# Kernel tuning notes

Hardware: AMD Instinct MI355X
Metric: run time of the kernel (lower is better)

## Reference

```python
import jax, jax.numpy as jnp
import numpy as np

N, E, D, ED, SH = 100000, 1600000, 64, 16, 9

# Real spherical harmonics l=0,1,2, 'integral' normalization (e3nn default),
# applied to unit direction vectors. Coefficients: 1/(2*sqrt(pi)), sqrt(3/4pi), etc.

def _sh(d):
    x, y, z = d[:, 0], d[:, 1], d[:, 2]
    return jnp.stack([
        jnp.full_like(x, 0.28209479177387814),          # l=0
        0.4886025119029199 * y,                          # l=1, m=-1
        0.4886025119029199 * z,                          # l=1, m=0
        0.4886025119029199 * x,                          # l=1, m=1
        1.0925484305920792 * x * y,                      # l=2, m=-2
        1.0925484305920792 * y * z,                      # l=2, m=-1
        0.31539156525252005 * (3.0 * z * z - 1.0),       # l=2, m=0
        1.0925484305920792 * x * z,                      # l=2, m=1
        0.5462742152960396 * (x * x - y * y),            # l=2, m=2
    ], axis=1)


def _mlp(h, W1, b1, W2, b2):  # Linear -> SiLU -> Linear
    return jax.nn.silu(h @ W1 + b1) @ W2 + b2


def setup_inputs() -> dict:
    key = jax.random.key(0)
    ks = jax.random.split(key, 16)
    def rn(k, shape, scale=0.05):
        return jax.random.normal(k, shape, dtype=jnp.float32) * scale
    return {
        "x": jax.random.normal(ks[0], (N, D), jnp.float32),
        "pos": jax.random.normal(ks[1], (N, 3), jnp.float32) * 3.0,
        "edge_attr": jax.random.normal(ks[2], (E, ED), jnp.float32),
        "row": jax.random.randint(ks[3], (E,), 0, N, dtype=jnp.int32),
        "col": jax.random.randint(ks[4], (E,), 0, N, dtype=jnp.int32),
        "node_W1": rn(ks[5], (D, D)), "node_b1": jnp.zeros((D,), jnp.float32),
        "node_W2": rn(ks[6], (D, D)), "node_b2": jnp.zeros((D,), jnp.float32),
        "edge_W1": rn(ks[7], (SH + ED, D)), "edge_b1": jnp.zeros((D,), jnp.float32),
        "edge_W2": rn(ks[8], (D, D)), "edge_b2": jnp.zeros((D,), jnp.float32),
        "out_W1": rn(ks[9], (2 * D, D)), "out_b1": jnp.zeros((D,), jnp.float32),
        "out_W2": rn(ks[10], (D, D)), "out_b2": jnp.zeros((D,), jnp.float32),
        "bn_gamma": jnp.ones((D,), jnp.float32), "bn_beta": jnp.zeros((D,), jnp.float32),
    }


def reference(x, pos, edge_attr, row, col,
              node_W1, node_b1, node_W2, node_b2,
              edge_W1, edge_b1, edge_W2, edge_b2,
              out_W1, out_b1, out_W2, out_b2,
              bn_gamma, bn_beta):
    # gather node positions per edge -> relative vectors
    rel = pos[row] - pos[col]                                    # [E,3]
    length = jnp.sqrt(jnp.sum(rel * rel, axis=1, keepdims=True) + 1e-12)
    d = rel / length
    d = d / (jnp.sqrt(jnp.sum(d * d, axis=1, keepdims=True)) + 1e-10)
    edge_sh = _sh(d)                                             # [E,9]
    edge_feat = jnp.concatenate([edge_sh, edge_attr], axis=1)    # [E,9+ED]
    x_t = _mlp(x, node_W1, node_b1, node_W2, node_b2)            # [N,D]
    e_w = _mlp(edge_feat, edge_W1, edge_b1, edge_W2, edge_b2)    # [E,D]
    msg = x_t[row] * e_w                                         # message = x_j * edge_attr
    # scatter-mean onto target nodes (edge_index[1] == col)
    s = jax.ops.segment_sum(msg, col, num_segments=N)            # [N,D]
    cnt = jax.ops.segment_sum(jnp.ones((E,), msg.dtype), col, num_segments=N)
    agg = s / jnp.maximum(cnt, 1.0)[:, None]
    h = jnp.concatenate([agg, x], axis=1)                        # [N,2D]
    h = _mlp(h, out_W1, out_b1, out_W2, out_b2)                  # [N,D]
    # BatchNorm over node dim (scalar irreps), training-mode batch stats
    mean = jnp.mean(h, axis=0)
    var = jnp.var(h, axis=0)
    return (h - mean) / jnp.sqrt(var + 1e-5) * bn_gamma + bn_beta
```

## Files before the change

kernel.cpp:

```cpp
#include <hip/hip_runtime.h>
#include <math.h>

#define DD 64
#define EDA 16

#define FR_E1 0
#define FR_E2 4
#define FR_N1 12
#define FR_N2 20
#define FR_O1 28
#define FR_O2 44
#define FR_TOT 52

#define PADH 72
#define PADF 68

#define HS 72

typedef unsigned int u32;
typedef unsigned long long u64;
typedef __attribute__((ext_vector_type(8))) short short8;
typedef __attribute__((ext_vector_type(4))) float f32x4;

static __device__ __forceinline__ float silu(float v) {
    return v / (1.0f + __expf(-v));
}
static __device__ __forceinline__ unsigned short f2bf(float f) {
    unsigned u = __float_as_uint(f);
    unsigned r = u + 0x7FFFu + ((u >> 16) & 1u);
    return (unsigned short)(r >> 16);
}
static __device__ __forceinline__ float bf2f(unsigned short u) {
    return __uint_as_float(((unsigned)u) << 16);
}
static __device__ __forceinline__ float bflo(u32 v) {
    return __uint_as_float(v << 16);
}
static __device__ __forceinline__ float bfhi(u32 v) {
    return __uint_as_float(v & 0xFFFF0000u);
}
static __device__ __forceinline__ unsigned cvt_pk_bf16(float lo, float hi) {
    unsigned r;
    asm("v_cvt_pk_bf16_f32 %0, %1, %2" : "=v"(r) : "v"(lo), "v"(hi));
    return r;
}
static __device__ __forceinline__ int bperm(int idx_lane, int v) {
    return __builtin_amdgcn_ds_bpermute(idx_lane << 2, v);
}
static __device__ __forceinline__ void wave_lds_fence() {
    asm volatile("s_waitcnt lgkmcnt(0)" ::: "memory");
    __builtin_amdgcn_sched_barrier(0);
}

__global__ __launch_bounds__(256) void k_pack_w(
    const float* __restrict__ eW1, const float* __restrict__ eW2,
    const float* __restrict__ nW1, const float* __restrict__ nW2,
    const float* __restrict__ oW1, const float* __restrict__ oW2,
    unsigned short* __restrict__ wpk)
{
    int t = threadIdx.x;
    int nt = t >> 6, l = t & 63;
    int kc = l >> 4, n0 = l & 15;

    #pragma unroll
    for (int j = 0; j < 8; ++j) {
        int k = kc*8 + j;
        int orig = (k < 16) ? (9 + k) : ((k < 25) ? (k - 16) : -1);
        float v = (orig >= 0) ? eW1[orig*DD + nt*16 + n0] : 0.0f;
        wpk[((size_t)((FR_E1 + nt)*64 + l))*8 + j] = f2bf(v);
    }
    #pragma unroll
    for (int s = 0; s < 2; ++s) {
        #pragma unroll
        for (int j = 0; j < 8; ++j) {
            int k = s*32 + kc*8 + j;
            wpk[((size_t)((FR_E2 + s*4 + nt)*64 + l))*8 + j] = f2bf(eW2[k*DD + nt*16 + n0]);
            wpk[((size_t)((FR_N1 + s*4 + nt)*64 + l))*8 + j] = f2bf(nW1[k*DD + nt*16 + n0]);
            wpk[((size_t)((FR_N2 + s*4 + nt)*64 + l))*8 + j] = f2bf(nW2[k*DD + nt*16 + n0]);
            wpk[((size_t)((FR_O2 + s*4 + nt)*64 + l))*8 + j] = f2bf(oW2[k*DD + nt*16 + n0]);
        }
    }
    #pragma unroll
    for (int s = 0; s < 4; ++s) {
        #pragma unroll
        for (int j = 0; j < 8; ++j) {
            int k = s*32 + kc*8 + j;
            wpk[((size_t)((FR_O1 + s*4 + nt)*64 + l))*8 + j] = f2bf(oW1[k*DD + nt*16 + n0]);
        }
    }
}

__global__ __launch_bounds__(256, 2) void k_node_hist(
    const float* __restrict__ x,
    const unsigned short* __restrict__ wpk,
    const float* __restrict__ b1, const float* __restrict__ b2,
    unsigned short* __restrict__ x_tb, int n, int nodeBlocks,
    const int* __restrict__ col, u32* __restrict__ cnt, int n_e)
{
    __shared__ __align__(16) unsigned short tile[4][16*PADH];
    const int tid  = threadIdx.x;

    if (blockIdx.x >= nodeBlocks) {
        int g = (blockIdx.x - nodeBlocks) * 256 + tid;
        int base = g * 4;
        if (base + 3 < n_e) {
            int4 c = ((const int4*)col)[g];
            atomicAdd(&cnt[c.x], 1u);
            atomicAdd(&cnt[c.y], 1u);
            atomicAdd(&cnt[c.z], 1u);
            atomicAdd(&cnt[c.w], 1u);
        } else {
            for (int e = base; e < n_e; ++e) atomicAdd(&cnt[col[e]], 1u);
        }
        return;
    }

    const int wv   = tid >> 6;
    const int lane = tid & 63;
    const int kc   = lane >> 4;
    const int n0   = lane & 15;
    const int rbase = kc * 4;

    const short8* fb = (const short8*)wpk;
    short8 bw1[2][4], bw2[2][4];
    #pragma unroll
    for (int s = 0; s < 2; ++s)
        #pragma unroll
        for (int nt = 0; nt < 4; ++nt) {
            bw1[s][nt] = fb[(FR_N1 + s*4 + nt)*64 + lane];
            bw2[s][nt] = fb[(FR_N2 + s*4 + nt)*64 + lane];
        }
    float b1v[4], b2v[4];
    #pragma unroll
    for (int nt = 0; nt < 4; ++nt) { b1v[nt] = b1[nt*16 + n0]; b2v[nt] = b2[nt*16 + n0]; }

    const int base = blockIdx.x*64 + wv*16;
    int rc = min(base + n0, n - 1);
    const float* xr = x + (size_t)rc * DD;

    short8 a[2];
    #pragma unroll
    for (int m = 0; m < 2; ++m) {
        float4 u0 = *(const float4*)(xr + m*32 + kc*8);
        float4 u1 = *(const float4*)(xr + m*32 + kc*8 + 4);
        unsigned* au = (unsigned*)&a[m];
        au[0] = cvt_pk_bf16(u0.x, u0.y);
        au[1] = cvt_pk_bf16(u0.z, u0.w);
        au[2] = cvt_pk_bf16(u1.x, u1.y);
        au[3] = cvt_pk_bf16(u1.z, u1.w);
    }

    f32x4 zz = {0.f, 0.f, 0.f, 0.f};
    f32x4 hacc[4] = {zz, zz, zz, zz};
    #pragma unroll
    for (int m = 0; m < 2; ++m)
        #pragma unroll
        for (int nt = 0; nt < 4; ++nt)
            hacc[nt] = __builtin_amdgcn_mfma_f32_16x16x32_bf16(a[m], bw1[m][nt], hacc[nt], 0, 0, 0);

    #pragma unroll
    for (int nt = 0; nt < 4; ++nt)
        #pragma unroll
        for (int r = 0; r < 4; ++r)
            tile[wv][(rbase + r)*PADH + nt*16 + n0] = f2bf(silu(hacc[nt][r] + b1v[nt]));
    __syncthreads();

    short8 a2_0 = *(const short8*)&tile[wv][n0*PADH +  0 + kc*8];
    short8 a2_1 = *(const short8*)&tile[wv][n0*PADH + 32 + kc*8];
    f32x4 oacc[4];
    #pragma unroll
    for (int nt = 0; nt < 4; ++nt) {
        oacc[nt] = __builtin_amdgcn_mfma_f32_16x16x32_bf16(a2_0, bw2[0][nt], zz, 0, 0, 0);
        oacc[nt] = __builtin_amdgcn_mfma_f32_16x16x32_bf16(a2_1, bw2[1][nt], oacc[nt], 0, 0, 0);
    }
    __syncthreads();

    #pragma unroll
    for (int nt = 0; nt < 4; ++nt)
        #pragma unroll
        for (int r = 0; r < 4; ++r)
            tile[wv][(rbase + r)*PADH + nt*16 + n0] = f2bf(oacc[nt][r] + b2v[nt]);
    __syncthreads();

    int ei = lane >> 2, q = lane & 3;
    int er = base + ei;
    if (er < n) {
        uint4* dst = (uint4*)(x_tb + (size_t)er * DD);
        dst[q]     = *(const uint4*)&tile[wv][ei*PADH + q*8];
        dst[q + 4] = *(const uint4*)&tile[wv][ei*PADH + (q + 4)*8];
    }
}

__global__ __launch_bounds__(256) void k_scan1(
    const u32* __restrict__ cnt, u32* __restrict__ bsum, int n)
{
    __shared__ u32 s[256];
    int i = blockIdx.x * 256 + threadIdx.x;
    s[threadIdx.x] = (i < n) ? cnt[i] : 0u;
    __syncthreads();
    for (int o = 128; o > 0; o >>= 1) {
        if (threadIdx.x < o) s[threadIdx.x] += s[threadIdx.x + o];
        __syncthreads();
    }
    if (threadIdx.x == 0) bsum[blockIdx.x] = s[0];
}

__global__ __launch_bounds__(512) void k_scan2(
    const u32* __restrict__ bsum, u32* __restrict__ boff, int nb)
{
    __shared__ u32 s[512];
    int t = threadIdx.x;
    u32 v = (t < nb) ? bsum[t] : 0u;
    s[t] = v;
    __syncthreads();
    for (int o = 1; o < 512; o <<= 1) {
        u32 a = (t >= o) ? s[t - o] : 0u;
        __syncthreads();
        s[t] += a;
        __syncthreads();
    }
    if (t < nb) boff[t] = s[t] - v;
}

__global__ __launch_bounds__(256) void k_scan3(
    const u32* __restrict__ cnt, const u32* __restrict__ boff,
    u32* __restrict__ wp, int n)
{
    __shared__ u32 s[256];
    int t = threadIdx.x;
    int i = blockIdx.x * 256 + t;
    u32 v = (i < n) ? cnt[i] : 0u;
    s[t] = v;
    __syncthreads();
    for (int o = 1; o < 256; o <<= 1) {
        u32 a = (t >= o) ? s[t - o] : 0u;
        __syncthreads();
        s[t] += a;
        __syncthreads();
    }
    if (i < n) wp[i] = boff[blockIdx.x] + s[t] - v;
}

__global__ __launch_bounds__(256) void k_scatter(
    const int* __restrict__ row, const int* __restrict__ col,
    u32* __restrict__ wp, u64* __restrict__ ce,
    float* __restrict__ agg, int n_agg4, int n_e)
{
    int e = blockIdx.x * 256 + threadIdx.x;
    if (e < n_agg4) {
        float4 z = {0.f, 0.f, 0.f, 0.f};
        ((float4*)agg)[e] = z;
    }
    if (e >= n_e) return;
    int c = col[e];
    int r = row[e];
    u32 p = atomicAdd(&wp[c], 1u);
    u32 lo = (u32)e | ((u32)r << 21);
    u32 hi = ((u32)r >> 11) | ((u32)c << 6);
    u64 pk = (u64)lo | ((u64)hi << 32);
    __builtin_nontemporal_store(pk, &ce[p]);
}

__global__ __launch_bounds__(256, 4) void k_edge_fused(
    const float* __restrict__ pos,
    const float* __restrict__ edge_attr,
    const u64* __restrict__ ce,
    const unsigned short* __restrict__ x_tb,
    const unsigned short* __restrict__ wpk,
    const float* __restrict__ b1, const float* __restrict__ b2,
    float* __restrict__ agg, int n_e)
{
    __shared__ __align__(16) unsigned short t_s[4][16*HS];
    __shared__ __align__(16) unsigned short wls[8*64*8];

    const int tid  = threadIdx.x;
    const int wv   = tid >> 6;
    const int lane = tid & 63;
    const int kc   = lane >> 4;
    const int n0   = lane & 15;

    {
        const uint4* wsrc = (const uint4*)(wpk + FR_E2*64*8);
        uint4* wdst = (uint4*)wls;
        wdst[tid*2]     = wsrc[tid*2];
        wdst[tid*2 + 1] = wsrc[tid*2 + 1];
    }

    const short8* fb = (const short8*)wpk;
    short8 bw1[4];
    #pragma unroll
    for (int nt = 0; nt < 4; ++nt) bw1[nt] = fb[(FR_E1 + nt)*64 + lane];

    uint2 bp1[4], bp2[4];
    #pragma unroll
    for (int nt = 0; nt < 4; ++nt) {
        float4 q1 = *(const float4*)(b1 + nt*16 + kc*4);
        float4 q2 = *(const float4*)(b2 + nt*16 + kc*4);
        bp1[nt].x = cvt_pk_bf16(q1.x, q1.y); bp1[nt].y = cvt_pk_bf16(q1.z, q1.w);
        bp2[nt].x = cvt_pk_bf16(q2.x, q2.y); bp2[nt].y = cvt_pk_bf16(q2.z, q2.w);
    }

    const int gbase = blockIdx.x*256 + wv*64;
    int g  = gbase + lane;
    int gc = min(g, n_e - 1);
    u64 pk = ce[gc];
    u32 pklo = (u32)pk, pkhi = (u32)(pk >> 32);
    int eo = (int)(pklo & 0x1FFFFFu);
    int rw = (int)((pklo >> 21) | ((pkhi & 0x3Fu) << 11));
    int cl = (int)(pkhi >> 6);

    float ax = pos[3*rw+0] - pos[3*cl+0];
    float ay = pos[3*rw+1] - pos[3*cl+1];
    float az = pos[3*rw+2] - pos[3*cl+2];
    float len = sqrtf(fmaf(ax,ax, fmaf(ay,ay, az*az)) + 1e-12f);
    float dx = ax/len, dy = ay/len, dz = az/len;
    float n2 = sqrtf(fmaf(dx,dx, fmaf(dy,dy, dz*dz)));
    float inv = 1.0f/(n2 + 1e-10f);
    dx *= inv; dy *= inv; dz *= inv;

    u32 shp01 = cvt_pk_bf16(0.28209479177387814f, 0.4886025119029199f*dy);
    u32 shp23 = cvt_pk_bf16(0.4886025119029199f*dz, 0.4886025119029199f*dx);
    u32 shp45 = cvt_pk_bf16(1.0925484305920792f*dx*dy, 1.0925484305920792f*dy*dz);
    u32 shp67 = cvt_pk_bf16(0.31539156525252005f*(3.0f*dz*dz - 1.0f),
                            1.0925484305920792f*dx*dz);
    u32 shp8  = cvt_pk_bf16(0.5462742152960396f*(dx*dx - dy*dy), 0.0f);

    int cln = bperm(min(lane + 1, 63), cl);
    u64 fmask = __ballot(cln != cl) | 0x8000800080008000ull;

    f32x4 zz = {0.f, 0.f, 0.f, 0.f};

    __syncthreads();

    #pragma unroll 1
    for (int tt = 0; tt < 4; ++tt) {
        const int le = tt*16 + n0;
        bool valid = (gbase + le) < n_e;

        int ea  = bperm(le, eo);
        int rv  = bperm(le, rw);
        u32 s01 = (u32)bperm(le, (int)shp01);
        u32 s23 = (u32)bperm(le, (int)shp23);
        u32 s45 = (u32)bperm(le, (int)shp45);
        u32 s67 = (u32)bperm(le, (int)shp67);
        u32 s8  = (u32)bperm(le, (int)shp8);

        const unsigned short* xrow = x_tb + (size_t)rv * DD;
        uint2 xv0 = *(const uint2*)(xrow +  0 + kc*4);
        uint2 xv1 = *(const uint2*)(xrow + 16 + kc*4);
        uint2 xv2 = *(const uint2*)(xrow + 32 + kc*4);
        uint2 xv3 = *(const uint2*)(xrow + 48 + kc*4);

        short8 af;
        unsigned* au = (unsigned*)&af;
        if (kc < 2) {
            const float4* ap = (const float4*)(edge_attr + (size_t)ea*EDA + kc*8);
            float4 a0 = ap[0], a1 = ap[1];
            au[0] = cvt_pk_bf16(a0.x, a0.y);
            au[1] = cvt_pk_bf16(a0.z, a0.w);
            au[2] = cvt_pk_bf16(a1.x, a1.y);
            au[3] = cvt_pk_bf16(a1.z, a1.w);
        } else if (kc == 2) {
            au[0] = s01; au[1] = s23; au[2] = s45; au[3] = s67;
        } else {
            au[0] = s8; au[1] = 0u; au[2] = 0u; au[3] = 0u;
        }

        f32x4 hacc[4];
        #pragma unroll
        for (int nt = 0; nt < 4; ++nt)
            hacc[nt] = __builtin_amdgcn_mfma_f32_16x16x32_bf16(bw1[nt], af, zz, 0, 0, 0);

        #pragma unroll
        for (int nt = 0; nt < 4; ++nt) {
            float h0 = silu(hacc[nt][0] + bflo(bp1[nt].x));
            float h1 = silu(hacc[nt][1] + bfhi(bp1[nt].x));
            float h2 = silu(hacc[nt][2] + bflo(bp1[nt].y));
            float h3 = silu(hacc[nt][3] + bfhi(bp1[nt].y));
            uint2 pr;
            pr.x = cvt_pk_bf16(h0, h1);
            pr.y = cvt_pk_bf16(h2, h3);
            *(uint2*)&t_s[wv][n0*HS + nt*16 + kc*4] = pr;
        }
        wave_lds_fence();

        short8 bf0 = *(const short8*)&t_s[wv][n0*HS +  0 + kc*8];
        short8 bf1 = *(const short8*)&t_s[wv][n0*HS + 32 + kc*8];
        f32x4 oacc[4];
        #pragma unroll
        for (int nt = 0; nt < 4; ++nt) {
            short8 w0 = *(const short8*)&wls[((0*4 + nt)*64 + lane)*8];
            oacc[nt] = __builtin_amdgcn_mfma_f32_16x16x32_bf16(w0, bf0, zz, 0, 0, 0);
            short8 w1 = *(const short8*)&wls[((1*4 + nt)*64 + lane)*8];
            oacc[nt] = __builtin_amdgcn_mfma_f32_16x16x32_bf16(w1, bf1, oacc[nt], 0, 0, 0);
        }

        if (!valid) {
            xv0.x = xv0.y = xv1.x = xv1.y = 0u;
            xv2.x = xv2.y = xv3.x = xv3.y = 0u;
        }
        {
            float m0, m1, m2, m3;
            uint2 pr;
            m0 = (oacc[0][0] + bflo(bp2[0].x)) * bflo(xv0.x);
            m1 = (oacc[0][1] + bfhi(bp2[0].x)) * bfhi(xv0.x);
            m2 = (oacc[0][2] + bflo(bp2[0].y)) * bflo(xv0.y);
            m3 = (oacc[0][3] + bfhi(bp2[0].y)) * bfhi(xv0.y);
            pr.x = cvt_pk_bf16(m0, m1); pr.y = cvt_pk_bf16(m2, m3);
            *(uint2*)&t_s[wv][n0*HS +  0 + kc*4] = pr;
            m0 = (oacc[1][0] + bflo(bp2[1].x)) * bflo(xv1.x);
            m1 = (oacc[1][1] + bfhi(bp2[1].x)) * bfhi(xv1.x);
            m2 = (oacc[1][2] + bflo(bp2[1].y)) * bflo(xv1.y);
            m3 = (oacc[1][3] + bfhi(bp2[1].y)) * bfhi(xv1.y);
            pr.x = cvt_pk_bf16(m0, m1); pr.y = cvt_pk_bf16(m2, m3);
            *(uint2*)&t_s[wv][n0*HS + 16 + kc*4] = pr;
            m0 = (oacc[2][0] + bflo(bp2[2].x)) * bflo(xv2.x);
            m1 = (oacc[2][1] + bfhi(bp2[2].x)) * bfhi(xv2.x);
            m2 = (oacc[2][2] + bflo(bp2[2].y)) * bflo(xv2.y);
            m3 = (oacc[2][3] + bfhi(bp2[2].y)) * bfhi(xv2.y);
            pr.x = cvt_pk_bf16(m0, m1); pr.y = cvt_pk_bf16(m2, m3);
            *(uint2*)&t_s[wv][n0*HS + 32 + kc*4] = pr;
            m0 = (oacc[3][0] + bflo(bp2[3].x)) * bflo(xv3.x);
            m1 = (oacc[3][1] + bfhi(bp2[3].x)) * bfhi(xv3.x);
            m2 = (oacc[3][2] + bflo(bp2[3].y)) * bflo(xv3.y);
            m3 = (oacc[3][3] + bfhi(bp2[3].y)) * bfhi(xv3.y);
            pr.x = cvt_pk_bf16(m0, m1); pr.y = cvt_pk_bf16(m2, m3);
            *(uint2*)&t_s[wv][n0*HS + 48 + kc*4] = pr;
        }
        wave_lds_fence();

        {
            float acc = 0.0f;
            #pragma unroll
            for (int r = 0; r < 16; ++r) {
                acc += bf2f(t_s[wv][r*HS + lane]);
                if ((fmask >> (tt*16 + r)) & 1ull) {
                    int cur = __builtin_amdgcn_readlane(cl, tt*16 + r);
                    unsafeAtomicAdd(&agg[(size_t)cur*DD + lane], acc);
                    acc = 0.0f;
                }
            }
        }
    }
}

__global__ __launch_bounds__(256, 2) void k_out_mfma(
    const float* __restrict__ agg, const u32* __restrict__ cnt,
    const float* __restrict__ x,
    const unsigned short* __restrict__ wpk,
    const float* __restrict__ b1, const float* __restrict__ b2,
    float* __restrict__ h, float* __restrict__ sums, int n)
{
    __shared__ __align__(16) unsigned short htile[4][16*PADH];
    __shared__ __align__(16) float otile[4][16*PADF];
    const int tid  = threadIdx.x;
    const int wv   = tid >> 6;
    const int lane = tid & 63;
    const int kc   = lane >> 4;
    const int n0   = lane & 15;
    const int rbase = kc * 4;

    const short8* fb = (const short8*)wpk;
    short8 bw1[4][4], bw2[2][4];
    #pragma unroll
    for (int s = 0; s < 4; ++s)
        #pragma unroll
        for (int nt = 0; nt < 4; ++nt) bw1[s][nt] = fb[(FR_O1 + s*4 + nt)*64 + lane];
    #pragma unroll
    for (int s = 0; s < 2; ++s)
        #pragma unroll
        for (int nt = 0; nt < 4; ++nt) bw2[s][nt] = fb[(FR_O2 + s*4 + nt)*64 + lane];

    float b1v[4], b2v[4];
    #pragma unroll
    for (int nt = 0; nt < 4; ++nt) { b1v[nt] = b1[nt*16 + n0]; b2v[nt] = b2[nt*16 + n0]; }

    const int base = blockIdx.x*64 + wv*16;
    int rc = min(base + n0, n - 1);
    const float* ar = agg + (size_t)rc * DD;
    const float* xr = x   + (size_t)rc * DD;
    float invc = 1.0f / fmaxf((float)cnt[rc], 1.0f);

    short8 a[4];
    #pragma unroll
    for (int m = 0; m < 4; ++m) {
        const float* src = (m < 2) ? (ar + m*32 + kc*8) : (xr + (m-2)*32 + kc*8);
        float4 u0 = *(const float4*)(src);
        float4 u1 = *(const float4*)(src + 4);
        if (m < 2) {
            u0.x*=invc; u0.y*=invc; u0.z*=invc; u0.w*=invc;
            u1.x*=invc; u1.y*=invc; u1.z*=invc; u1.w*=invc;
        }
        unsigned* au = (unsigned*)&a[m];
        au[0] = cvt_pk_bf16(u0.x, u0.y);
        au[1] = cvt_pk_bf16(u0.z, u0.w);
        au[2] = cvt_pk_bf16(u1.x, u1.y);
        au[3] = cvt_pk_bf16(u1.z, u1.w);
    }

    f32x4 zz = {0.f, 0.f, 0.f, 0.f};
    f32x4 hacc[4] = {zz, zz, zz, zz};
    #pragma unroll
    for (int m = 0; m < 4; ++m)
        #pragma unroll
        for (int nt = 0; nt < 4; ++nt)
            hacc[nt] = __builtin_amdgcn_mfma_f32_16x16x32_bf16(a[m], bw1[m][nt], hacc[nt], 0, 0, 0);

    #pragma unroll
    for (int nt = 0; nt < 4; ++nt)
        #pragma unroll
        for (int r = 0; r < 4; ++r)
            htile[wv][(rbase + r)*PADH + nt*16 + n0] = f2bf(silu(hacc[nt][r] + b1v[nt]));
    __syncthreads();

    short8 a2_0 = *(const short8*)&htile[wv][n0*PADH +  0 + kc*8];
    short8 a2_1 = *(const short8*)&htile[wv][n0*PADH + 32 + kc*8];
    f32x4 oacc[4];
    #pragma unroll
    for (int nt = 0; nt < 4; ++nt) {
        oacc[nt] = __builtin_amdgcn_mfma_f32_16x16x32_bf16(a2_0, bw2[0][nt], zz, 0, 0, 0);
        oacc[nt] = __builtin_amdgcn_mfma_f32_16x16x32_bf16(a2_1, bw2[1][nt], oacc[nt], 0, 0, 0);
    }

    #pragma unroll
    for (int nt = 0; nt < 4; ++nt)
        #pragma unroll
        for (int r = 0; r < 4; ++r)
            otile[wv][(rbase + r)*PADF + nt*16 + n0] = oacc[nt][r] + b2v[nt];
    __syncthreads();

    int ei = lane >> 2, q = lane & 3;
    int er = base + ei;
    if (er < n) {
        float4* dst = (float4*)(h + (size_t)er * DD);
        #pragma unroll
        for (int k = 0; k < 4; ++k)
            dst[q + 4*k] = *(const float4*)&otile[wv][ei*PADF + (q + 4*k)*4];
    }

    if (tid < 64) {
        int f = tid;
        float s = 0.f, qq = 0.f;
        #pragma unroll
        for (int w = 0; w < 4; ++w) {
            int base_w = blockIdx.x*64 + w*16;
            int nv = n - base_w;
            nv = nv < 0 ? 0 : (nv > 16 ? 16 : nv);
            for (int r = 0; r < nv; ++r) {
                float v = otile[w][r*PADF + f];
                s += v; qq = fmaf(v, v, qq);
            }
        }
        unsafeAtomicAdd(&sums[f], s);
        unsafeAtomicAdd(&sums[DD + f], qq);
    }
}

__global__ __launch_bounds__(256) void k_bn_norm(
    float* __restrict__ h, const float* __restrict__ sums,
    const float* __restrict__ gamma, const float* __restrict__ beta,
    float inv_n, int total4)
{
    int g = blockIdx.x*256 + threadIdx.x;
    if (g >= total4) return;
    int f0 = (g*4) & (DD-1);
    float4 v = ((const float4*)h)[g];
    float4 sm = *(const float4*)(sums + f0);
    float4 sq = *(const float4*)(sums + DD + f0);
    float4 gm = *(const float4*)(gamma + f0);
    float4 bt = *(const float4*)(beta + f0);
    float m0 = sm.x*inv_n, m1 = sm.y*inv_n, m2 = sm.z*inv_n, m3 = sm.w*inv_n;
    float s0 = gm.x * rsqrtf(sq.x*inv_n - m0*m0 + 1e-5f);
    float s1 = gm.y * rsqrtf(sq.y*inv_n - m1*m1 + 1e-5f);
    float s2 = gm.z * rsqrtf(sq.z*inv_n - m2*m2 + 1e-5f);
    float s3 = gm.w * rsqrtf(sq.w*inv_n - m3*m3 + 1e-5f);
    v.x = fmaf(v.x - m0, s0, bt.x);
    v.y = fmaf(v.y - m1, s1, bt.y);
    v.z = fmaf(v.z - m2, s2, bt.z);
    v.w = fmaf(v.w - m3, s3, bt.w);
    ((float4*)h)[g] = v;
}

static inline size_t al16(size_t v) { return (v + 15) & ~(size_t)15; }

extern "C" void kernel_launch(void* const* d_in, const int* in_sizes, int n_in,
                              void* d_out, int out_size, void* d_ws, size_t ws_size,
                              hipStream_t stream)
{
    const float* x         = (const float*)d_in[0];
    const float* pos       = (const float*)d_in[1];
    const float* edge_attr = (const float*)d_in[2];
    const int*   row       = (const int*)d_in[3];
    const int*   col       = (const int*)d_in[4];
    const float* nW1 = (const float*)d_in[5];
    const float* nb1 = (const float*)d_in[6];
    const float* nW2 = (const float*)d_in[7];
    const float* nb2 = (const float*)d_in[8];
    const float* eW1 = (const float*)d_in[9];
    const float* eb1 = (const float*)d_in[10];
    const float* eW2 = (const float*)d_in[11];
    const float* eb2 = (const float*)d_in[12];
    const float* oW1 = (const float*)d_in[13];
    const float* ob1 = (const float*)d_in[14];
    const float* oW2 = (const float*)d_in[15];
    const float* ob2 = (const float*)d_in[16];
    const float* gamma = (const float*)d_in[17];
    const float* beta  = (const float*)d_in[18];

    const int N = in_sizes[0] / DD;
    const int E = in_sizes[3];
    const int NB = (N + 255) / 256;
    const int nodeBlocks = (N + 63) / 64;
    const int histBlocks = (E/4 + 255) / 256;

    float* hout = (float*)d_out;
    char* ws = (char*)d_ws;

    size_t o_xtb  = 0;
    size_t o_cnt  = o_xtb  + (size_t)N*DD*2;
    size_t o_sums = o_cnt  + (size_t)N*4;
    size_t o_agg  = o_sums + 128*4;
    size_t o_wp   = o_agg  + (size_t)N*DD*4;
    size_t o_bsum = o_wp   + (size_t)N*4;
    size_t o_boff = al16(o_bsum + (size_t)NB*4);
    size_t o_wpk  = al16(o_boff + (size_t)NB*4);
    size_t o_ce   = al16(o_wpk + (size_t)FR_TOT*64*8*2);
    size_t need   = o_ce + (size_t)E*8;

    if (ws_size < need) return;

    unsigned short* x_tb = (unsigned short*)(ws + o_xtb);
    u32*   cnt  = (u32*)(ws + o_cnt);
    float* sums = (float*)(ws + o_sums);
    float* agg  = (float*)(ws + o_agg);
    u32*   wp   = (u32*)(ws + o_wp);
    u32*   bsum = (u32*)(ws + o_bsum);
    u32*   boff = (u32*)(ws + o_boff);
    unsigned short* wpk = (unsigned short*)(ws + o_wpk);
    u64*   ce   = (u64*)(ws + o_ce);

    hipMemsetAsync(cnt, 0, (size_t)N*4 + 128*4, stream);

    k_pack_w<<<1, 256, 0, stream>>>(eW1, eW2, nW1, nW2, oW1, oW2, wpk);
    k_node_hist<<<nodeBlocks + histBlocks, 256, 0, stream>>>(
        x, wpk, nb1, nb2, x_tb, N, nodeBlocks, col, cnt, E);
    k_scan1<<<NB, 256, 0, stream>>>(cnt, bsum, N);
    k_scan2<<<1, 512, 0, stream>>>(bsum, boff, NB);
    k_scan3<<<NB, 256, 0, stream>>>(cnt, boff, wp, N);
    k_scatter<<<(E + 255)/256, 256, 0, stream>>>(row, col, wp, ce, agg, N*DD/4, E);
    k_edge_fused<<<(E + 255)/256, 256, 0, stream>>>(pos, edge_attr, ce, x_tb,
                                                    wpk, eb1, eb2, agg, E);
    k_out_mfma<<<(N + 63)/64, 256, 0, stream>>>(agg, cnt, x, wpk, ob1, ob2, hout, sums, N);
    k_bn_norm<<<(N*DD/4 + 255)/256, 256, 0, stream>>>(hout, sums, gamma, beta,
                                                      1.0f/(float)N, N*DD/4);
}
```

Before: 337.8 us.

## Collapse scan kernels into one atomic-offset scan, fold memset into pack kernel

Replaces the three-kernel exclusive scan with a single kernel in which each block claims its base offset from a global atomic counter. The resulting segment offsets are not in node order, which is acceptable for bucketing edges by destination. The memset is folded into the weight-pack kernel as extra zeroing blocks, removing launches and serialization. The x_t row layout is permuted so the edge kernel can read each node row with two 16-byte loads instead of four 8-byte loads. The node kernel's occupancy hint is also raised to 3 blocks per multiprocessor.

```diff
diff --git a/kernel.cpp b/kernel.cpp
--- a/kernel.cpp
+++ b/kernel.cpp
@@ -52,12 +52,18 @@
     __builtin_amdgcn_sched_barrier(0);
 }
 
-__global__ __launch_bounds__(256) void k_pack_w(
+__global__ __launch_bounds__(256) void k_pack_zero(
     const float* __restrict__ eW1, const float* __restrict__ eW2,
     const float* __restrict__ nW1, const float* __restrict__ nW2,
     const float* __restrict__ oW1, const float* __restrict__ oW2,
-    unsigned short* __restrict__ wpk)
-{
+    unsigned short* __restrict__ wpk,
+    uint4* __restrict__ zbase, int nz4)
+{
+    if (blockIdx.x > 0) {
+        int i = (blockIdx.x - 1) * 256 + threadIdx.x;
+        if (i < nz4) zbase[i] = make_uint4(0u, 0u, 0u, 0u);
+        return;
+    }
     int t = threadIdx.x;
     int nt = t >> 6, l = t & 63;
     int kc = l >> 4, n0 = l & 15;
@@ -90,7 +96,7 @@
     }
 }
 
-__global__ __launch_bounds__(256, 2) void k_node_hist(
+__global__ __launch_bounds__(256, 3) void k_node_hist(
     const float* __restrict__ x,
     const unsigned short* __restrict__ wpk,
     const float* __restrict__ b1, const float* __restrict__ b2,
@@ -179,7 +185,8 @@
     for (int nt = 0; nt < 4; ++nt)
         #pragma unroll
         for (int r = 0; r < 4; ++r)
-            tile[wv][(rbase + r)*PADH + nt*16 + n0] = f2bf(oacc[nt][r] + b2v[nt]);
+            tile[wv][(rbase + r)*PADH + (n0>>2)*16 + nt*4 + (n0&3)] =
+                f2bf(oacc[nt][r] + b2v[nt]);
     __syncthreads();
 
     int ei = lane >> 2, q = lane & 3;
@@ -191,42 +198,12 @@
     }
 }
 
-__global__ __launch_bounds__(256) void k_scan1(
-    const u32* __restrict__ cnt, u32* __restrict__ bsum, int n)
+__global__ __launch_bounds__(256) void k_scan_bump(
+    const u32* __restrict__ cnt, u32* __restrict__ wp,
+    u32* __restrict__ gctr, int n)
 {
     __shared__ u32 s[256];
-    int i = blockIdx.x * 256 + threadIdx.x;
-    s[threadIdx.x] = (i < n) ? cnt[i] : 0u;
-    __syncthreads();
-    for (int o = 128; o > 0; o >>= 1) {
-        if (threadIdx.x < o) s[threadIdx.x] += s[threadIdx.x + o];
-        __syncthreads();
-    }
-    if (threadIdx.x == 0) bsum[blockIdx.x] = s[0];
-}
-
-__global__ __launch_bounds__(512) void k_scan2(
-    const u32* __restrict__ bsum, u32* __restrict__ boff, int nb)
-{
-    __shared__ u32 s[512];
-    int t = threadIdx.x;
-    u32 v = (t < nb) ? bsum[t] : 0u;
-    s[t] = v;
-    __syncthreads();
-    for (int o = 1; o < 512; o <<= 1) {
-        u32 a = (t >= o) ? s[t - o] : 0u;
-        __syncthreads();
-        s[t] += a;
-        __syncthreads();
-    }
-    if (t < nb) boff[t] = s[t] - v;
-}
-
-__global__ __launch_bounds__(256) void k_scan3(
-    const u32* __restrict__ cnt, const u32* __restrict__ boff,
-    u32* __restrict__ wp, int n)
-{
-    __shared__ u32 s[256];
+    __shared__ u32 base;
     int t = threadIdx.x;
     int i = blockIdx.x * 256 + t;
     u32 v = (i < n) ? cnt[i] : 0u;
@@ -238,7 +215,9 @@
         s[t] += a;
         __syncthreads();
     }
-    if (i < n) wp[i] = boff[blockIdx.x] + s[t] - v;
+    if (t == 255) base = atomicAdd(gctr, s[255]);
+    __syncthreads();
+    if (i < n) wp[i] = base + s[t] - v;
 }
 
 __global__ __launch_bounds__(256) void k_scatter(
@@ -345,11 +324,11 @@
         u32 s67 = (u32)bperm(le, (int)shp67);
         u32 s8  = (u32)bperm(le, (int)shp8);
 
-        const unsigned short* xrow = x_tb + (size_t)rv * DD;
-        uint2 xv0 = *(const uint2*)(xrow +  0 + kc*4);
-        uint2 xv1 = *(const uint2*)(xrow + 16 + kc*4);
-        uint2 xv2 = *(const uint2*)(xrow + 32 + kc*4);
-        uint2 xv3 = *(const uint2*)(xrow + 48 + kc*4);
+        const unsigned short* xrow = x_tb + (size_t)rv * DD + kc*16;
+        uint4 qa = *(const uint4*)(xrow);
+        uint4 qb = *(const uint4*)(xrow + 8);
+        uint2 xv0 = {qa.x, qa.y}, xv1 = {qa.z, qa.w};
+        uint2 xv2 = {qb.x, qb.y}, xv3 = {qb.z, qb.w};
 
         short8 af;
         unsigned* au = (unsigned*)&af;
@@ -619,11 +598,10 @@
     size_t o_xtb  = 0;
     size_t o_cnt  = o_xtb  + (size_t)N*DD*2;
     size_t o_sums = o_cnt  + (size_t)N*4;
-    size_t o_agg  = o_sums + 128*4;
+    size_t o_gctr = o_sums + 128*4;
+    size_t o_agg  = o_gctr + 16;
     size_t o_wp   = o_agg  + (size_t)N*DD*4;
-    size_t o_bsum = o_wp   + (size_t)N*4;
-    size_t o_boff = al16(o_bsum + (size_t)NB*4);
-    size_t o_wpk  = al16(o_boff + (size_t)NB*4);
+    size_t o_wpk  = al16(o_wp + (size_t)N*4);
     size_t o_ce   = al16(o_wpk + (size_t)FR_TOT*64*8*2);
     size_t need   = o_ce + (size_t)E*8;
 
@@ -632,21 +610,20 @@
     unsigned short* x_tb = (unsigned short*)(ws + o_xtb);
     u32*   cnt  = (u32*)(ws + o_cnt);
     float* sums = (float*)(ws + o_sums);
+    u32*   gctr = (u32*)(ws + o_gctr);
     float* agg  = (float*)(ws + o_agg);
     u32*   wp   = (u32*)(ws + o_wp);
-    u32*   bsum = (u32*)(ws + o_bsum);
-    u32*   boff = (u32*)(ws + o_boff);
     unsigned short* wpk = (unsigned short*)(ws + o_wpk);
     u64*   ce   = (u64*)(ws + o_ce);
 
-    hipMemsetAsync(cnt, 0, (size_t)N*4 + 128*4, stream);
-
-    k_pack_w<<<1, 256, 0, stream>>>(eW1, eW2, nW1, nW2, oW1, oW2, wpk);
+    const int nz4 = (N + 132 + 3) / 4;
+    const int zBlocks = (nz4 + 255) / 256;
+
+    k_pack_zero<<<1 + zBlocks, 256, 0, stream>>>(eW1, eW2, nW1, nW2, oW1, oW2, wpk,
+                                                 (uint4*)cnt, nz4);
     k_node_hist<<<nodeBlocks + histBlocks, 256, 0, stream>>>(
         x, wpk, nb1, nb2, x_tb, N, nodeBlocks, col, cnt, E);
-    k_scan1<<<NB, 256, 0, stream>>>(cnt, bsum, N);
-    k_scan2<<<1, 512, 0, stream>>>(bsum, boff, NB);
-    k_scan3<<<NB, 256, 0, stream>>>(cnt, boff, wp, N);
+    k_scan_bump<<<NB, 256, 0, stream>>>(cnt, wp, gctr, N);
     k_scatter<<<(E + 255)/256, 256, 0, stream>>>(row, col, wp, ce, agg, N*DD/4, E);
     k_edge_fused<<<(E + 255)/256, 256, 0, stream>>>(pos, edge_attr, ce, x_tb,
                                                     wpk, eb1, eb2, agg, E);
```

Measured after the change: 327.2 us (median of 2 runs). 1.03x faster.
